# Performance work log

Hardware: AMD Instinct MI355X
Metric: run time of the kernel (lower is better)

Reference implementation:

```python
import itertools
import jax, jax.numpy as jnp
import numpy as np

N_QUBITS = 8
N_LAYERS = 2
BATCH = 8192
INPUT_DIM = 3072
NUM_CLASSES = 10

_In = np.eye(2, dtype=np.complex64)
_Xn = np.array([[0, 1], [1, 0]], dtype=np.complex64)
_Yn = np.array([[0, -1j], [1j, 0]], dtype=np.complex64)
_Zn = np.array([[1, 0], [0, -1]], dtype=np.complex64)
_P = {"I": _In, "X": _Xn, "Y": _Yn, "Z": _Zn}
_XX = jnp.asarray(np.kron(_Xn, _Xn))
_YY = jnp.asarray(np.kron(_Yn, _Yn))
_ZZ = jnp.asarray(np.kron(_Zn, _Zn))
_I4 = jnp.eye(4, dtype=jnp.complex64)
# 2-qubit Pauli words in PennyLane ArbitraryUnitary order: IX, IY, IZ, XI, ..., ZZ
_WORDS = jnp.asarray(np.stack([np.kron(_P[a], _P[b]) for a, b in itertools.product("IXYZ", repeat=2)][1:]))


def apply_gate(state, U, wires):
    """Apply a 2^k x 2^k gate U to the given wires of a (2,)*n statevector."""
    n = state.ndim
    k = len(wires)
    U = U.reshape((2,) * (2 * k)).astype(state.dtype)
    state = jnp.tensordot(U, state, axes=(list(range(k, 2 * k)), list(wires)))
    rest = [a for a in range(n) if a not in wires]
    perm = [0] * n
    for i, a in enumerate(wires):
        perm[a] = i
    for j, a in enumerate(rest):
        perm[a] = k + j
    return jnp.transpose(state, perm)


def u3_mat(t, p, d):
    ct, st = jnp.cos(t / 2).astype(jnp.complex64), jnp.sin(t / 2).astype(jnp.complex64)
    r0 = jnp.stack([ct, -jnp.exp(1j * d) * st])
    r1 = jnp.stack([jnp.exp(1j * p) * st, jnp.exp(1j * (p + d)) * ct])
    return jnp.stack([r0, r1])


def ry_mat(t):
    c, s = jnp.cos(t / 2), jnp.sin(t / 2)
    return jnp.stack([jnp.stack([c, -s]), jnp.stack([s, c])]).astype(jnp.complex64)


def ising_mat(phi, pauli2):
    # exp(-i phi/2 P) for two-qubit Pauli word P (P^2 = I)
    return jnp.cos(phi / 2) * _I4 - 1j * jnp.sin(phi / 2) * pauli2


def circuit(conv_w, pool_w, last_w, feats):
    state = jnp.zeros((2,) * N_QUBITS, jnp.complex64).at[(0,) * N_QUBITS].set(1.0)
    # AngleEmbedding with RY rotations
    for w in range(N_QUBITS):
        state = apply_gate(state, ry_mat(feats[w]), (w,))
    wires = list(range(N_QUBITS))
    for layer in range(N_LAYERS):
        cw = conv_w[layer]
        nw = len(wires)
        for p in (0, 1):
            for idx in range(nw - 1):
                if idx % 2 == p:
                    a, b = wires[idx], wires[idx + 1]
                    state = apply_gate(state, u3_mat(cw[idx, 0], cw[idx, 1], cw[idx, 2]), (a,))
                    state = apply_gate(state, u3_mat(cw[idx + 1, 3], cw[idx + 1, 4], cw[idx + 1, 5]), (b,))
                    state = apply_gate(state, ising_mat(cw[idx, 6], _ZZ), (a, b))
                    state = apply_gate(state, ising_mat(cw[idx, 7], _YY), (a, b))
                    state = apply_gate(state, ising_mat(cw[idx, 8], _XX), (a, b))
                    state = apply_gate(state, u3_mat(cw[idx, 9], cw[idx, 10], cw[idx, 11]), (a,))
                    state = apply_gate(state, u3_mat(cw[idx + 1, 12], cw[idx + 1, 13], cw[idx + 1, 14]), (b,))
        # Pooling: mid-circuit measure + conditional U3 == (deferred measurement)
        pw = pool_w[layer]
        for idx in range(1, nw, 2):
            u = u3_mat(pw[idx // 2, 0], pw[idx // 2, 1], pw[idx // 2, 2])
            cu = jnp.zeros((4, 4), jnp.complex64).at[0, 0].set(1.0).at[1, 1].set(1.0).at[2:, 2:].set(u)
            state = apply_gate(state, cu, (wires[idx], wires[idx - 1]))
        wires = wires[::2]
    # ArbitraryUnitary on remaining 2 wires: product of 15 PauliRot gates
    for k in range(15):
        mat = jnp.cos(last_w[k] / 2) * _I4 - 1j * jnp.sin(last_w[k] / 2) * _WORDS[k]
        state = apply_gate(state, mat, tuple(wires))
    probs = state.real ** 2 + state.imag ** 2
    z = jnp.sum(probs, axis=tuple(range(1, N_QUBITS)))  # (2,)
    return z[0] - z[1]


def setup_inputs() -> dict:
    key = jax.random.key(0)
    ks = jax.random.split(key, 8)
    return {
        "x": jax.random.normal(ks[0], (BATCH, INPUT_DIM), jnp.float32),
        "fc_w": jax.random.normal(ks[1], (N_QUBITS, INPUT_DIM), jnp.float32) * 0.02,
        "fc_b": jnp.zeros((N_QUBITS,), jnp.float32),
        "conv_params": jax.random.normal(ks[2], (N_LAYERS, N_QUBITS, 15), jnp.float32),
        "pool_params": jax.random.normal(ks[3], (N_LAYERS, N_QUBITS // 2, 3), jnp.float32),
        "last_params": jax.random.normal(ks[4], (15,), jnp.float32),
        "out_w": jax.random.normal(ks[5], (NUM_CLASSES, 1), jnp.float32),
        "out_b": jnp.zeros((NUM_CLASSES,), jnp.float32),
    }


def reference(x, fc_w, fc_b, conv_params, pool_params, last_params, out_w, out_b):
    feats = jnp.tanh(x.reshape(x.shape[0], -1) @ fc_w.T + fc_b)  # (B, n_qubits)
    qvals = jax.vmap(lambda f: circuit(conv_params, pool_params, last_params, f))(feats)
    logits = qvals[:, None].astype(x.dtype) @ out_w.T + out_b  # (B, num_classes)
    return logits
```

## Files before the change

kernel.cpp:

```cpp
#include <hip/hip_runtime.h>
#include <math.h>

__constant__ int G_ORD[17] = {0,1,2,3,4,5,6, 10,11,12,13, 7,8,9, 14,15, 16};
__constant__ int G_WA[17]  = {0,2,4,6,1,3,5, 1,3,5,7, 0,4,2, 2,6, 0};
__constant__ int G_WB[17]  = {1,3,5,7,2,4,6, 0,2,4,6, 2,6,4, 0,4, 4};
__constant__ int CDESC[10][3] = {{0,0,1},{0,2,3},{0,4,5},{0,6,7},{0,1,2},{0,3,4},{0,5,6},
                                 {1,0,1},{1,2,3},{1,1,2}};
__constant__ int PDESC[6][2] = {{0,0},{0,1},{0,2},{0,3},{1,0},{1,1}};
__constant__ float2 PMAT[4][4] = {
  {{1.f,0.f},{0.f,0.f},{0.f,0.f},{1.f,0.f}},
  {{0.f,0.f},{1.f,0.f},{1.f,0.f},{0.f,0.f}},
  {{0.f,0.f},{0.f,-1.f},{0.f,1.f},{0.f,0.f}},
  {{1.f,0.f},{0.f,0.f},{0.f,0.f},{-1.f,0.f}}};

__device__ __forceinline__ float2 cmul(float2 a, float2 b){
  return make_float2(a.x*b.x - a.y*b.y, a.x*b.y + a.y*b.x);
}
__device__ __forceinline__ float2 cadd(float2 a, float2 b){
  return make_float2(a.x+b.x, a.y+b.y);
}

__device__ void u3m(float t, float p, float d, float2* u){
  float ct = cosf(0.5f*t), st = sinf(0.5f*t);
  u[0] = make_float2(ct, 0.f);
  u[1] = make_float2(-cosf(d)*st, -sinf(d)*st);
  u[2] = make_float2(cosf(p)*st,  sinf(p)*st);
  u[3] = make_float2(cosf(p+d)*ct, sinf(p+d)*ct);
}

__global__ __launch_bounds__(320) void build_gates_kernel(
    const float* __restrict__ conv, const float* __restrict__ pool,
    const float* __restrict__ last, float2* __restrict__ G){
  __shared__ float2 gm[2][17][16];
  int t = threadIdx.x;
  int g = t >> 4, e = t & 15, r = e >> 2, c = e & 3;
  float2 A1[4], B1[4], A2[4], B2[4];
  int nsteps = 0;
  if (g < 10){
    int layer = CDESC[g][0], ra = CDESC[g][1], rb = CDESC[g][2];
    const float* cw = conv + layer*120;
    int bA = ra*15, bB = rb*15;
    u3m(cw[bA+0],  cw[bA+1],  cw[bA+2],  A1);
    u3m(cw[bB+3],  cw[bB+4],  cw[bB+5],  B1);
    u3m(cw[bA+9],  cw[bA+10], cw[bA+11], A2);
    u3m(cw[bB+12], cw[bB+13], cw[bB+14], B2);
    nsteps = 5;
  } else if (g < 16){
    nsteps = 1;
  } else if (g == 16){
    nsteps = 16;
  }
  for (int s = 0; s < 16; s++){
    if (g < 17 && s < nsteps){
      float2 T = make_float2(0.f, 0.f);
      if (g < 10){
        if (s == 0){
          T = cmul(A1[(r>>1)*2 + (c>>1)], B1[(r&1)*2 + (c&1)]);
        } else if (s <= 3){
          int layer = CDESC[g][0], ra = CDESC[g][1];
          float phi = conv[layer*120 + ra*15 + 5 + s];
          int q_ = 4 - s;
          float ch = cosf(0.5f*phi), sh = sinf(0.5f*phi);
          #pragma unroll
          for (int k=0;k<4;k++){
            float2 w = cmul(PMAT[q_][(r>>1)*2 + (k>>1)], PMAT[q_][(r&1)*2 + (k&1)]);
            float2 rk = make_float2(sh*w.y, -sh*w.x);
            if (k == r) rk.x += ch;
            T = cadd(T, cmul(rk, gm[s&1][g][k*4 + c]));
          }
        } else {
          #pragma unroll
          for (int k=0;k<4;k++){
            float2 k2 = cmul(A2[(r>>1)*2 + (k>>1)], B2[(r&1)*2 + (k&1)]);
            T = cadd(T, cmul(k2, gm[s&1][g][k*4 + c]));
          }
        }
      } else if (g < 16){
        int layer = PDESC[g-10][0], h = PDESC[g-10][1];
        const float* pw = pool + layer*12 + h*3;
        float2 u[4];
        u3m(pw[0], pw[1], pw[2], u);
        if (e == 0 || e == 5) T = make_float2(1.f, 0.f);
        else if (e == 10) T = u[0];
        else if (e == 11) T = u[1];
        else if (e == 14) T = u[2];
        else if (e == 15) T = u[3];
      } else {
        if (s == 0){
          T = make_float2((r==c)?1.f:0.f, 0.f);
        } else {
          int w_ = s;
          int qa = w_ >> 2, qb = w_ & 3;
          float phi = last[s-1];
          float ch = cosf(0.5f*phi), sh = sinf(0.5f*phi);
          #pragma unroll
          for (int k=0;k<4;k++){
            float2 w = cmul(PMAT[qa][(r>>1)*2 + (k>>1)], PMAT[qb][(r&1)*2 + (k&1)]);
            float2 rk = make_float2(sh*w.y, -sh*w.x);
            if (k == r) rk.x += ch;
            T = cadd(T, cmul(rk, gm[s&1][16][k*4 + c]));
          }
        }
      }
      gm[(s+1)&1][g][e] = T;
      if (s == nsteps-1) G[g*16 + e] = T;
    }
    __syncthreads();
  }
}

__global__ __launch_bounds__(64) void build_u_kernel(
    const float2* __restrict__ G, float2* __restrict__ U){
  __shared__ float2 gl[17][16];
  __shared__ float2 st[256];
  int t = threadIdx.x, col = blockIdx.x;
  float2* glf = (float2*)gl;
  for (int k=t; k<272; k+=64) glf[k] = G[k];
  #pragma unroll
  for (int k=t; k<256; k+=64) st[k] = make_float2(k==col ? 1.f : 0.f, 0.f);
  __syncthreads();
  for (int g=0; g<17; g++){
    int slot = G_ORD[g];
    float2 m[16];
    #pragma unroll
    for (int i=0;i<16;i++) m[i] = gl[slot][i];
    int pa = 7 - G_WA[g], pb = 7 - G_WB[g];
    int plo = pa < pb ? pa : pb, phi_ = pa < pb ? pb : pa;
    int mm = t;
    int t1   = ((mm >> plo) << (plo+1)) | (mm & ((1<<plo)-1));
    int base = ((t1 >> phi_) << (phi_+1)) | (t1 & ((1<<phi_)-1));
    int ba = 1<<pa, bb = 1<<pb;
    int i0 = base, i1 = base|bb, i2 = base|ba, i3 = base|ba|bb;
    float2 s0 = st[i0], s1 = st[i1], s2 = st[i2], s3 = st[i3];
    float2 n0 = cadd(cadd(cmul(m[0], s0), cmul(m[1], s1)), cadd(cmul(m[2], s2), cmul(m[3], s3)));
    float2 n1 = cadd(cadd(cmul(m[4], s0), cmul(m[5], s1)), cadd(cmul(m[6], s2), cmul(m[7], s3)));
    float2 n2 = cadd(cadd(cmul(m[8], s0), cmul(m[9], s1)), cadd(cmul(m[10],s2), cmul(m[11],s3)));
    float2 n3 = cadd(cadd(cmul(m[12],s0), cmul(m[13],s1)), cadd(cmul(m[14],s2), cmul(m[15],s3)));
    st[i0] = n0; st[i1] = n1; st[i2] = n2; st[i3] = n3;
    __syncthreads();
  }
  #pragma unroll
  for (int k=t; k<256; k+=64) U[k*256 + col] = st[k];
}

__global__ __launch_bounds__(256) void build_a_kernel(
    const float2* __restrict__ U, float* __restrict__ A){
  int j = threadIdx.x, i = blockIdx.x;
  float a = 0.f;
  #pragma unroll 8
  for (int k=0; k<256; k++){
    float2 uj = U[k*256 + j];
    float2 ui = U[k*256 + i];
    float sgn = (k < 128) ? 1.f : -1.f;
    a += sgn*(ui.x*uj.x + ui.y*uj.y);
  }
  A[i*256 + j] = a;
}

__global__ __launch_bounds__(256, 4) void main_kernel(
    const float* __restrict__ x, const float* __restrict__ fcw,
    const float* __restrict__ fcb, const float* __restrict__ Ag,
    const float* __restrict__ outw, const float* __restrict__ outb,
    float* __restrict__ out){
  __shared__ float lds[10240];
  float* red  = lds;
  float* As   = lds;
  float* ps   = lds + 8192;
  float* flds = lds + 8192;
  int t = threadIdx.x, lane = t & 63, wv = t >> 6, jb = lane;
  int r0 = blockIdx.x * 8;
  {
    int rw = r0 + wv*2;
    const float4* x4 = (const float4*)x;
    const float4* w4 = (const float4*)fcw;
    float acc[2][8];
    #pragma unroll
    for (int r=0;r<2;r++)
      #pragma unroll
      for (int o=0;o<8;o++) acc[r][o] = 0.f;
    #pragma unroll 2
    for (int p=0; p<12; p++){
      float4 wf[8];
      #pragma unroll
      for (int o=0;o<8;o++) wf[o] = w4[o*768 + p*64 + lane];
      #pragma unroll
      for (int r=0;r<2;r++){
        float4 xv = x4[(size_t)(rw+r)*768 + p*64 + lane];
        #pragma unroll
        for (int o=0;o<8;o++){
          acc[r][o] += xv.x*wf[o].x + xv.y*wf[o].y + xv.z*wf[o].z + xv.w*wf[o].w;
        }
      }
    }
    #pragma unroll
    for (int r=0;r<2;r++)
      #pragma unroll
      for (int o=0;o<8;o++)
        red[((wv*2+r)*8 + o)*68 + lane] = acc[r][o];
  }
  __syncthreads();
  if (t < 64){
    const float4* rp = (const float4*)(red + t*68);
    float4 s4 = make_float4(0.f,0.f,0.f,0.f);
    #pragma unroll
    for (int i=0;i<16;i++){
      float4 v = rp[i];
      s4.x += v.x; s4.y += v.y; s4.z += v.z; s4.w += v.w;
    }
    flds[t] = tanhf(s4.x + s4.y + s4.z + s4.w + fcb[t & 7]);
  }
  __syncthreads();
  float psi_local[16];
  if (t < 128){
    int row = t >> 4, i1 = t & 15;
    float fv[8];
    #pragma unroll
    for (int w=0; w<8; w++) fv[w] = flds[row*8 + w];
    float cc[8], ss[8];
    #pragma unroll
    for (int w=0; w<8; w++){
      float a = 0.5f*fv[w];
      __sincosf(a, &ss[w], &cc[w]);
    }
    float Hv = (i1&8 ? ss[0]:cc[0]) * (i1&4 ? ss[1]:cc[1])
             * (i1&2 ? ss[2]:cc[2]) * (i1&1 ? ss[3]:cc[3]);
    float l2[2], l4[4], l8[8], L[16];
    l2[0]=cc[4]; l2[1]=ss[4];
    #pragma unroll
    for (int a=0;a<2;a++){ l4[a*2]=l2[a]*cc[5]; l4[a*2+1]=l2[a]*ss[5]; }
    #pragma unroll
    for (int a=0;a<4;a++){ l8[a*2]=l4[a]*cc[6]; l8[a*2+1]=l4[a]*ss[6]; }
    #pragma unroll
    for (int a=0;a<8;a++){ L[a*2]=l8[a]*cc[7]; L[a*2+1]=l8[a]*ss[7]; }
    #pragma unroll
    for (int j=0;j<16;j++) psi_local[j] = Hv*L[j];
  }
  __syncthreads();
  if (t < 128){
    int row = t >> 4, i1 = t & 15;
    float4* dst = (float4*)(ps + row*256 + i1*16);
    #pragma unroll
    for (int qd=0; qd<4; qd++)
      dst[qd] = make_float4(psi_local[qd*4+0], psi_local[qd*4+1],
                            psi_local[qd*4+2], psi_local[qd*4+3]);
  }
  const float4* As4 = (const float4*)As;
  const float4* ps4 = (const float4*)ps;
  const float4* Ag4 = (const float4*)Ag;
  float4 acc4[2];
  #pragma unroll
  for (int r=0;r<2;r++) acc4[r] = make_float4(0.f,0.f,0.f,0.f);
  for (int chunk=0; chunk<8; chunk++){
    __syncthreads();
    #pragma unroll
    for (int pass=0; pass<8; pass++){
      int kk = pass*4 + wv;
      *(float4*)(As + kk*256 + jb*4) = Ag4[(chunk*32 + kk)*64 + jb];
    }
    __syncthreads();
    #pragma unroll
    for (int kq=0; kq<8; kq++){
      float4 av0 = As4[(kq*4+0)*64 + jb];
      float4 av1 = As4[(kq*4+1)*64 + jb];
      float4 av2 = As4[(kq*4+2)*64 + jb];
      float4 av3 = As4[(kq*4+3)*64 + jb];
      #pragma unroll
      for (int r=0; r<2; r++){
        float4 pv = ps4[(wv*2+r)*64 + chunk*8 + kq];
        acc4[r].x += pv.x*av0.x + pv.y*av1.x + pv.z*av2.x + pv.w*av3.x;
        acc4[r].y += pv.x*av0.y + pv.y*av1.y + pv.z*av2.y + pv.w*av3.y;
        acc4[r].z += pv.x*av0.z + pv.y*av1.z + pv.z*av2.z + pv.w*av3.z;
        acc4[r].w += pv.x*av0.w + pv.y*av1.w + pv.z*av2.w + pv.w*av3.w;
      }
    }
  }
  float p[2];
  #pragma unroll
  for (int r=0; r<2; r++){
    float4 psv = ps4[(wv*2+r)*64 + jb];
    float pr = acc4[r].x*psv.x + acc4[r].y*psv.y + acc4[r].z*psv.z + acc4[r].w*psv.w;
    #pragma unroll
    for (int m=1; m<64; m<<=1) pr += __shfl_xor(pr, m, 64);
    p[r] = pr;
  }
  if (jb < 20){
    int ridx = jb / 10, c = jb - ridx*10;
    float q = (ridx==0) ? p[0] : p[1];
    out[(r0 + wv*2 + ridx)*10 + c] = q*outw[c] + outb[c];
  }
}

extern "C" void kernel_launch(void* const* d_in, const int* in_sizes, int n_in,
                              void* d_out, int out_size, void* d_ws, size_t ws_size,
                              hipStream_t stream) {
  const float* x    = (const float*)d_in[0];
  const float* fcw  = (const float*)d_in[1];
  const float* fcb  = (const float*)d_in[2];
  const float* conv = (const float*)d_in[3];
  const float* pool = (const float*)d_in[4];
  const float* last = (const float*)d_in[5];
  const float* outw = (const float*)d_in[6];
  const float* outb = (const float*)d_in[7];
  float* out = (float*)d_out;

  float* ws = (float*)d_ws;
  float2* U  = (float2*)ws;
  float*  Am = ws + 131072;
  float2* G  = (float2*)(ws + 131072);

  build_gates_kernel<<<1, 320, 0, stream>>>(conv, pool, last, G);
  build_u_kernel<<<256, 64, 0, stream>>>(G, U);
  build_a_kernel<<<256, 256, 0, stream>>>(U, Am);
  main_kernel<<<1024, 256, 0, stream>>>(x, fcw, fcb, Am, outw, outb, out);
}
```

Baseline: 256.8 us.

## Fuse gate building into U kernel and split quadratic form over K per wave

Gate matrix construction is folded into the per-column U builder, so each of the 256 blocks recomputes the 17 gates redundantly and one kernel launch disappears. The main kernel no longer stages A through LDS in chunks with barriers. Each wave now reads its quarter of A's rows straight from global/L2 and accumulates all 8 batch rows, with a small LDS cross-wave reduction at the end. This cuts LDS use and barriers at the cost of more accumulator registers and redundant gate math.

```diff
diff --git a/kernel.cpp b/kernel.cpp
--- a/kernel.cpp
+++ b/kernel.cpp
@@ -28,119 +28,114 @@
   u[3] = make_float2(cosf(p+d)*ct, sinf(p+d)*ct);
 }
 
-__global__ __launch_bounds__(320) void build_gates_kernel(
+__global__ __launch_bounds__(320) void build_u_kernel(
     const float* __restrict__ conv, const float* __restrict__ pool,
-    const float* __restrict__ last, float2* __restrict__ G){
+    const float* __restrict__ last, float2* __restrict__ U){
   __shared__ float2 gm[2][17][16];
-  int t = threadIdx.x;
-  int g = t >> 4, e = t & 15, r = e >> 2, c = e & 3;
-  float2 A1[4], B1[4], A2[4], B2[4];
-  int nsteps = 0;
-  if (g < 10){
-    int layer = CDESC[g][0], ra = CDESC[g][1], rb = CDESC[g][2];
-    const float* cw = conv + layer*120;
-    int bA = ra*15, bB = rb*15;
-    u3m(cw[bA+0],  cw[bA+1],  cw[bA+2],  A1);
-    u3m(cw[bB+3],  cw[bB+4],  cw[bB+5],  B1);
-    u3m(cw[bA+9],  cw[bA+10], cw[bA+11], A2);
-    u3m(cw[bB+12], cw[bB+13], cw[bB+14], B2);
-    nsteps = 5;
-  } else if (g < 16){
-    nsteps = 1;
-  } else if (g == 16){
-    nsteps = 16;
-  }
-  for (int s = 0; s < 16; s++){
-    if (g < 17 && s < nsteps){
-      float2 T = make_float2(0.f, 0.f);
-      if (g < 10){
-        if (s == 0){
-          T = cmul(A1[(r>>1)*2 + (c>>1)], B1[(r&1)*2 + (c&1)]);
-        } else if (s <= 3){
-          int layer = CDESC[g][0], ra = CDESC[g][1];
-          float phi = conv[layer*120 + ra*15 + 5 + s];
-          int q_ = 4 - s;
-          float ch = cosf(0.5f*phi), sh = sinf(0.5f*phi);
-          #pragma unroll
-          for (int k=0;k<4;k++){
-            float2 w = cmul(PMAT[q_][(r>>1)*2 + (k>>1)], PMAT[q_][(r&1)*2 + (k&1)]);
-            float2 rk = make_float2(sh*w.y, -sh*w.x);
-            if (k == r) rk.x += ch;
-            T = cadd(T, cmul(rk, gm[s&1][g][k*4 + c]));
-          }
-        } else {
-          #pragma unroll
-          for (int k=0;k<4;k++){
-            float2 k2 = cmul(A2[(r>>1)*2 + (k>>1)], B2[(r&1)*2 + (k&1)]);
-            T = cadd(T, cmul(k2, gm[s&1][g][k*4 + c]));
-          }
-        }
-      } else if (g < 16){
-        int layer = PDESC[g-10][0], h = PDESC[g-10][1];
-        const float* pw = pool + layer*12 + h*3;
-        float2 u[4];
-        u3m(pw[0], pw[1], pw[2], u);
-        if (e == 0 || e == 5) T = make_float2(1.f, 0.f);
-        else if (e == 10) T = u[0];
-        else if (e == 11) T = u[1];
-        else if (e == 14) T = u[2];
-        else if (e == 15) T = u[3];
-      } else {
-        if (s == 0){
-          T = make_float2((r==c)?1.f:0.f, 0.f);
-        } else {
-          int w_ = s;
-          int qa = w_ >> 2, qb = w_ & 3;
-          float phi = last[s-1];
-          float ch = cosf(0.5f*phi), sh = sinf(0.5f*phi);
-          #pragma unroll
-          for (int k=0;k<4;k++){
-            float2 w = cmul(PMAT[qa][(r>>1)*2 + (k>>1)], PMAT[qb][(r&1)*2 + (k&1)]);
-            float2 rk = make_float2(sh*w.y, -sh*w.x);
-            if (k == r) rk.x += ch;
-            T = cadd(T, cmul(rk, gm[s&1][16][k*4 + c]));
-          }
-        }
-      }
-      gm[(s+1)&1][g][e] = T;
-      if (s == nsteps-1) G[g*16 + e] = T;
-    }
-    __syncthreads();
-  }
-}
-
-__global__ __launch_bounds__(64) void build_u_kernel(
-    const float2* __restrict__ G, float2* __restrict__ U){
   __shared__ float2 gl[17][16];
   __shared__ float2 st[256];
   int t = threadIdx.x, col = blockIdx.x;
-  float2* glf = (float2*)gl;
-  for (int k=t; k<272; k+=64) glf[k] = G[k];
-  #pragma unroll
-  for (int k=t; k<256; k+=64) st[k] = make_float2(k==col ? 1.f : 0.f, 0.f);
+  {
+    int g = t >> 4, e = t & 15, r = e >> 2, c = e & 3;
+    float2 A1[4], B1[4], A2[4], B2[4];
+    int nsteps = 0;
+    if (g < 10){
+      int layer = CDESC[g][0], ra = CDESC[g][1], rb = CDESC[g][2];
+      const float* cw = conv + layer*120;
+      int bA = ra*15, bB = rb*15;
+      u3m(cw[bA+0],  cw[bA+1],  cw[bA+2],  A1);
+      u3m(cw[bB+3],  cw[bB+4],  cw[bB+5],  B1);
+      u3m(cw[bA+9],  cw[bA+10], cw[bA+11], A2);
+      u3m(cw[bB+12], cw[bB+13], cw[bB+14], B2);
+      nsteps = 5;
+    } else if (g < 16){
+      nsteps = 1;
+    } else if (g == 16){
+      nsteps = 16;
+    }
+    for (int s = 0; s < 16; s++){
+      if (g < 17 && s < nsteps){
+        float2 T = make_float2(0.f, 0.f);
+        if (g < 10){
+          if (s == 0){
+            T = cmul(A1[(r>>1)*2 + (c>>1)], B1[(r&1)*2 + (c&1)]);
+          } else if (s <= 3){
+            int layer = CDESC[g][0], ra = CDESC[g][1];
+            float phi = conv[layer*120 + ra*15 + 5 + s];
+            int q_ = 4 - s;
+            float ch = cosf(0.5f*phi), sh = sinf(0.5f*phi);
+            #pragma unroll
+            for (int k=0;k<4;k++){
+              float2 w = cmul(PMAT[q_][(r>>1)*2 + (k>>1)], PMAT[q_][(r&1)*2 + (k&1)]);
+              float2 rk = make_float2(sh*w.y, -sh*w.x);
+              if (k == r) rk.x += ch;
+              T = cadd(T, cmul(rk, gm[s&1][g][k*4 + c]));
+            }
+          } else {
+            #pragma unroll
+            for (int k=0;k<4;k++){
+              float2 k2 = cmul(A2[(r>>1)*2 + (k>>1)], B2[(r&1)*2 + (k&1)]);
+              T = cadd(T, cmul(k2, gm[s&1][g][k*4 + c]));
+            }
+          }
+        } else if (g < 16){
+          int layer = PDESC[g-10][0], h = PDESC[g-10][1];
+          const float* pw = pool + layer*12 + h*3;
+          float2 u[4];
+          u3m(pw[0], pw[1], pw[2], u);
+          if (e == 0 || e == 5) T = make_float2(1.f, 0.f);
+          else if (e == 10) T = u[0];
+          else if (e == 11) T = u[1];
+          else if (e == 14) T = u[2];
+          else if (e == 15) T = u[3];
+        } else {
+          if (s == 0){
+            T = make_float2((r==c)?1.f:0.f, 0.f);
+          } else {
+            int w_ = s;
+            int qa = w_ >> 2, qb = w_ & 3;
+            float phi = last[s-1];
+            float ch = cosf(0.5f*phi), sh = sinf(0.5f*phi);
+            #pragma unroll
+            for (int k=0;k<4;k++){
+              float2 w = cmul(PMAT[qa][(r>>1)*2 + (k>>1)], PMAT[qb][(r&1)*2 + (k&1)]);
+              float2 rk = make_float2(sh*w.y, -sh*w.x);
+              if (k == r) rk.x += ch;
+              T = cadd(T, cmul(rk, gm[s&1][16][k*4 + c]));
+            }
+          }
+        }
+        gm[(s+1)&1][g][e] = T;
+        if (s == nsteps-1) gl[g][e] = T;
+      }
+      __syncthreads();
+    }
+  }
+  if (t < 256) st[t] = make_float2(t==col ? 1.f : 0.f, 0.f);
   __syncthreads();
   for (int g=0; g<17; g++){
-    int slot = G_ORD[g];
-    float2 m[16];
-    #pragma unroll
-    for (int i=0;i<16;i++) m[i] = gl[slot][i];
-    int pa = 7 - G_WA[g], pb = 7 - G_WB[g];
-    int plo = pa < pb ? pa : pb, phi_ = pa < pb ? pb : pa;
-    int mm = t;
-    int t1   = ((mm >> plo) << (plo+1)) | (mm & ((1<<plo)-1));
-    int base = ((t1 >> phi_) << (phi_+1)) | (t1 & ((1<<phi_)-1));
-    int ba = 1<<pa, bb = 1<<pb;
-    int i0 = base, i1 = base|bb, i2 = base|ba, i3 = base|ba|bb;
-    float2 s0 = st[i0], s1 = st[i1], s2 = st[i2], s3 = st[i3];
-    float2 n0 = cadd(cadd(cmul(m[0], s0), cmul(m[1], s1)), cadd(cmul(m[2], s2), cmul(m[3], s3)));
-    float2 n1 = cadd(cadd(cmul(m[4], s0), cmul(m[5], s1)), cadd(cmul(m[6], s2), cmul(m[7], s3)));
-    float2 n2 = cadd(cadd(cmul(m[8], s0), cmul(m[9], s1)), cadd(cmul(m[10],s2), cmul(m[11],s3)));
-    float2 n3 = cadd(cadd(cmul(m[12],s0), cmul(m[13],s1)), cadd(cmul(m[14],s2), cmul(m[15],s3)));
-    st[i0] = n0; st[i1] = n1; st[i2] = n2; st[i3] = n3;
+    if (t < 64){
+      int slot = G_ORD[g];
+      float2 m[16];
+      #pragma unroll
+      for (int i=0;i<16;i++) m[i] = gl[slot][i];
+      int pa = 7 - G_WA[g], pb = 7 - G_WB[g];
+      int plo = pa < pb ? pa : pb, phi_ = pa < pb ? pb : pa;
+      int mm = t;
+      int t1   = ((mm >> plo) << (plo+1)) | (mm & ((1<<plo)-1));
+      int base = ((t1 >> phi_) << (phi_+1)) | (t1 & ((1<<phi_)-1));
+      int ba = 1<<pa, bb = 1<<pb;
+      int i0 = base, i1 = base|bb, i2 = base|ba, i3 = base|ba|bb;
+      float2 s0 = st[i0], s1 = st[i1], s2 = st[i2], s3 = st[i3];
+      float2 n0 = cadd(cadd(cmul(m[0], s0), cmul(m[1], s1)), cadd(cmul(m[2], s2), cmul(m[3], s3)));
+      float2 n1 = cadd(cadd(cmul(m[4], s0), cmul(m[5], s1)), cadd(cmul(m[6], s2), cmul(m[7], s3)));
+      float2 n2 = cadd(cadd(cmul(m[8], s0), cmul(m[9], s1)), cadd(cmul(m[10],s2), cmul(m[11],s3)));
+      float2 n3 = cadd(cadd(cmul(m[12],s0), cmul(m[13],s1)), cadd(cmul(m[14],s2), cmul(m[15],s3)));
+      st[i0] = n0; st[i1] = n1; st[i2] = n2; st[i3] = n3;
+    }
     __syncthreads();
   }
-  #pragma unroll
-  for (int k=t; k<256; k+=64) U[k*256 + col] = st[k];
+  if (t < 256) U[t*256 + col] = st[t];
 }
 
 __global__ __launch_bounds__(256) void build_a_kernel(
@@ -162,11 +157,11 @@
     const float* __restrict__ fcb, const float* __restrict__ Ag,
     const float* __restrict__ outw, const float* __restrict__ outb,
     float* __restrict__ out){
-  __shared__ float lds[10240];
-  float* red  = lds;
-  float* As   = lds;
-  float* ps   = lds + 8192;
-  float* flds = lds + 8192;
+  __shared__ float lds[6528];
+  float* ps    = lds;
+  float* flds  = lds + 2048;
+  float* pqred = lds + 2112;
+  float* red   = lds + 2176;
   int t = threadIdx.x, lane = t & 63, wv = t >> 6, jb = lane;
   int r0 = blockIdx.x * 8;
   {
@@ -210,7 +205,6 @@
     flds[t] = tanhf(s4.x + s4.y + s4.z + s4.w + fcb[t & 7]);
   }
   __syncthreads();
-  float psi_local[16];
   if (t < 128){
     int row = t >> 4, i1 = t & 15;
     float fv[8];
@@ -232,61 +226,53 @@
     for (int a=0;a<4;a++){ l8[a*2]=l4[a]*cc[6]; l8[a*2+1]=l4[a]*ss[6]; }
     #pragma unroll
     for (int a=0;a<8;a++){ L[a*2]=l8[a]*cc[7]; L[a*2+1]=l8[a]*ss[7]; }
-    #pragma unroll
-    for (int j=0;j<16;j++) psi_local[j] = Hv*L[j];
-  }
-  __syncthreads();
-  if (t < 128){
-    int row = t >> 4, i1 = t & 15;
     float4* dst = (float4*)(ps + row*256 + i1*16);
     #pragma unroll
     for (int qd=0; qd<4; qd++)
-      dst[qd] = make_float4(psi_local[qd*4+0], psi_local[qd*4+1],
-                            psi_local[qd*4+2], psi_local[qd*4+3]);
-  }
-  const float4* As4 = (const float4*)As;
+      dst[qd] = make_float4(Hv*L[qd*4+0], Hv*L[qd*4+1],
+                            Hv*L[qd*4+2], Hv*L[qd*4+3]);
+  }
+  __syncthreads();
   const float4* ps4 = (const float4*)ps;
   const float4* Ag4 = (const float4*)Ag;
-  float4 acc4[2];
+  float4 acc4[8];
   #pragma unroll
-  for (int r=0;r<2;r++) acc4[r] = make_float4(0.f,0.f,0.f,0.f);
-  for (int chunk=0; chunk<8; chunk++){
-    __syncthreads();
-    #pragma unroll
-    for (int pass=0; pass<8; pass++){
-      int kk = pass*4 + wv;
-      *(float4*)(As + kk*256 + jb*4) = Ag4[(chunk*32 + kk)*64 + jb];
-    }
-    __syncthreads();
-    #pragma unroll
-    for (int kq=0; kq<8; kq++){
-      float4 av0 = As4[(kq*4+0)*64 + jb];
-      float4 av1 = As4[(kq*4+1)*64 + jb];
-      float4 av2 = As4[(kq*4+2)*64 + jb];
-      float4 av3 = As4[(kq*4+3)*64 + jb];
-      #pragma unroll
-      for (int r=0; r<2; r++){
-        float4 pv = ps4[(wv*2+r)*64 + chunk*8 + kq];
-        acc4[r].x += pv.x*av0.x + pv.y*av1.x + pv.z*av2.x + pv.w*av3.x;
-        acc4[r].y += pv.x*av0.y + pv.y*av1.y + pv.z*av2.y + pv.w*av3.y;
-        acc4[r].z += pv.x*av0.z + pv.y*av1.z + pv.z*av2.z + pv.w*av3.z;
-        acc4[r].w += pv.x*av0.w + pv.y*av1.w + pv.z*av2.w + pv.w*av3.w;
-      }
-    }
-  }
-  float p[2];
+  for (int r=0;r<8;r++) acc4[r] = make_float4(0.f,0.f,0.f,0.f);
+  int kbase = wv*16;
+  #pragma unroll 2
+  for (int kq=0; kq<16; kq++){
+    int grp = kbase + kq;
+    float4 av0 = Ag4[(grp*4+0)*64 + jb];
+    float4 av1 = Ag4[(grp*4+1)*64 + jb];
+    float4 av2 = Ag4[(grp*4+2)*64 + jb];
+    float4 av3 = Ag4[(grp*4+3)*64 + jb];
+    #pragma unroll
+    for (int r=0; r<8; r++){
+      float4 pv = ps4[r*64 + grp];
+      acc4[r].x += pv.x*av0.x + pv.y*av1.x + pv.z*av2.x + pv.w*av3.x;
+      acc4[r].y += pv.x*av0.y + pv.y*av1.y + pv.z*av2.y + pv.w*av3.y;
+      acc4[r].z += pv.x*av0.z + pv.y*av1.z + pv.z*av2.z + pv.w*av3.z;
+      acc4[r].w += pv.x*av0.w + pv.y*av1.w + pv.z*av2.w + pv.w*av3.w;
+    }
+  }
+  float p[8];
   #pragma unroll
-  for (int r=0; r<2; r++){
-    float4 psv = ps4[(wv*2+r)*64 + jb];
+  for (int r=0; r<8; r++){
+    float4 psv = ps4[r*64 + jb];
     float pr = acc4[r].x*psv.x + acc4[r].y*psv.y + acc4[r].z*psv.z + acc4[r].w*psv.w;
     #pragma unroll
     for (int m=1; m<64; m<<=1) pr += __shfl_xor(pr, m, 64);
     p[r] = pr;
   }
-  if (jb < 20){
-    int ridx = jb / 10, c = jb - ridx*10;
-    float q = (ridx==0) ? p[0] : p[1];
-    out[(r0 + wv*2 + ridx)*10 + c] = q*outw[c] + outb[c];
+  if (jb == 0){
+    #pragma unroll
+    for (int r=0; r<8; r++) pqred[wv*8 + r] = p[r];
+  }
+  __syncthreads();
+  if (t < 80){
+    int row = t / 10, c = t - row*10;
+    float q = (pqred[row] + pqred[8 + row]) + (pqred[16 + row] + pqred[24 + row]);
+    out[(r0 + row)*10 + c] = q*outw[c] + outb[c];
   }
 }
 
@@ -306,10 +292,8 @@
   float* ws = (float*)d_ws;
   float2* U  = (float2*)ws;
   float*  Am = ws + 131072;
-  float2* G  = (float2*)(ws + 131072);
-
-  build_gates_kernel<<<1, 320, 0, stream>>>(conv, pool, last, G);
-  build_u_kernel<<<256, 64, 0, stream>>>(G, U);
+
+  build_u_kernel<<<256, 320, 0, stream>>>(conv, pool, last, U);
   build_a_kernel<<<256, 256, 0, stream>>>(U, Am);
   main_kernel<<<1024, 256, 0, stream>>>(x, fcw, fcb, Am, outw, outb, out);
 }
```

Measured after the change: 248.2 us. 1.03x faster.
